# Optimization experiments

Hardware: AMD Instinct MI355X
Metric: run time of the kernel (lower is better)

Reference implementation:

```python
import jax, jax.numpy as jnp
import numpy as np

N = 100000
E = 1600000
F_IN = 128
H = 128
G = 256  # number of graphs
EPS = 1e-5


def setup_inputs() -> dict:
    key = jax.random.key(0)
    ks = jax.random.split(key, 16)
    x = jax.random.normal(ks[0], (N, F_IN), dtype=jnp.float32)
    edge_index = jax.random.randint(ks[1], (2, E), 0, N, dtype=jnp.int64)
    batch = jnp.sort(jax.random.randint(ks[2], (N,), 0, G, dtype=jnp.int64))
    def glorot(k, shape):
        lim = float(np.sqrt(6.0 / (shape[0] + shape[1])))
        return jax.random.uniform(k, shape, jnp.float32, -lim, lim)
    inp = {
        "x": x, "edge_index": edge_index, "batch": batch,
        "W1": glorot(ks[3], (F_IN, H)), "b1": jnp.zeros((H,), jnp.float32),
        "g1": jnp.ones((H,), jnp.float32), "be1": jnp.zeros((H,), jnp.float32),
        "W2": glorot(ks[4], (H, H)), "b2": jnp.zeros((H,), jnp.float32),
        "g2": jnp.ones((H,), jnp.float32), "be2": jnp.zeros((H,), jnp.float32),
        "W3": glorot(ks[5], (H, H)), "b3": jnp.zeros((H,), jnp.float32),
        "g3": jnp.ones((H,), jnp.float32), "be3": jnp.zeros((H,), jnp.float32),
        "Wl": glorot(ks[6], (H, 1)), "bl": jnp.zeros((1,), jnp.float32),
    }
    return inp


def _gcn_precompute(edge_index):
    # add self-loops, compute symmetric norm coefficients (PyG GCNConv default)
    src = jnp.concatenate([edge_index[0], jnp.arange(N, dtype=edge_index.dtype)])
    dst = jnp.concatenate([edge_index[1], jnp.arange(N, dtype=edge_index.dtype)])
    deg = jax.ops.segment_sum(jnp.ones_like(dst, dtype=jnp.float32), dst, num_segments=N)
    dinv = jnp.where(deg > 0, deg ** -0.5, 0.0)
    coef = dinv[src] * dinv[dst]  # [E+N]
    return src, dst, coef


def _gcn_conv(x, src, dst, coef, W, b):
    h = x @ W                                  # [N, H] small GEMM
    msg = h[src] * coef[:, None]               # gather + scale over edges
    out = jax.ops.segment_sum(msg, dst, num_segments=N)  # scatter-add
    return out + b


def _batchnorm(x, g, be):
    # training-mode BN: batch statistics, biased variance (PyTorch semantics)
    mean = jnp.mean(x, axis=0)
    var = jnp.mean(jnp.square(x - mean), axis=0)
    return g * (x - mean) * jax.lax.rsqrt(var + EPS) + be


def reference(x, edge_index, batch, W1, b1, g1, be1, W2, b2, g2, be2,
              W3, b3, g3, be3, Wl, bl):
    src, dst, coef = _gcn_precompute(edge_index)
    h = _gcn_conv(x, src, dst, coef, W1, b1)
    h = jax.nn.relu(_batchnorm(h, g1, be1))  # dropout is identity in eval
    h = _gcn_conv(h, src, dst, coef, W2, b2)
    h = jax.nn.relu(_batchnorm(h, g2, be2))
    h = _gcn_conv(h, src, dst, coef, W3, b3)
    h = jax.nn.relu(_batchnorm(h, g3, be3))
    # global mean pool per graph
    sums = jax.ops.segment_sum(h, batch, num_segments=G)
    cnt = jax.ops.segment_sum(jnp.ones((N,), jnp.float32), batch, num_segments=G)
    pooled = sums / jnp.maximum(cnt, 1.0)[:, None]  # [G, H]
    return pooled @ Wl + bl                          # [G, 1]
```

## Files before the change

### kernel.cpp

```cpp
#include <hip/hip_runtime.h>
#include <hip/hip_bf16.h>

#define N_NODES 100000
#define E_EDGES 1600000
#define FDIM 128
#define NGRAPH 256
#define NPB 256
#define NBUCKET 391
#define SLAB 4800
#define BCHUNK 16384
#define NBINBLK ((E_EDGES + BCHUNK - 1) / BCHUNK)
#define LDSW 136
#define SREP 16

typedef __attribute__((ext_vector_type(8))) short bf16x8;
typedef __attribute__((ext_vector_type(4))) float f32x4;

__device__ __forceinline__ unsigned pack_bf16(float a, float b) {
    unsigned ua = __float_as_uint(a);
    unsigned ub = __float_as_uint(b);
    ua = ua + 0x7fffu + ((ua >> 16) & 1u);
    ub = ub + 0x7fffu + ((ub >> 16) & 1u);
    return (ua >> 16) | (ub & 0xffff0000u);
}
__device__ __forceinline__ unsigned short bf16_1(float a) {
    unsigned ua = __float_as_uint(a);
    ua = ua + 0x7fffu + ((ua >> 16) & 1u);
    return (unsigned short)(ua >> 16);
}
__device__ __forceinline__ float bf_lo(unsigned u) { return __uint_as_float(u << 16); }
__device__ __forceinline__ float bf_hi(unsigned u) { return __uint_as_float(u & 0xffff0000u); }


__global__ void initk(float* __restrict__ statsP, float* __restrict__ sums,
                      int* __restrict__ cursor) {
    int i = blockIdx.x * blockDim.x + threadIdx.x;
    if (i < 3 * SREP * 256) statsP[i] = 0.0f;
    if (i < NGRAPH * FDIM) sums[i] = 0.0f;
    if (i < NBUCKET) cursor[i] = i * SLAB;
}

__global__ __launch_bounds__(256) void bink(const int* __restrict__ ei,
                                            int* __restrict__ cursor,
                                            int* __restrict__ bcsr) {
    __shared__ int hist[NBUCKET];
    __shared__ int base[NBUCKET];
    int t = threadIdx.x;
    for (int b = t; b < NBUCKET; b += 256) hist[b] = 0;
    __syncthreads();
    int e0 = blockIdx.x * BCHUNK;
    int e1 = e0 + BCHUNK; if (e1 > E_EDGES) e1 = E_EDGES;
    for (int e = e0 + t; e < e1; e += 256) {
        atomicAdd(&hist[ei[E_EDGES + e] >> 8], 1);
    }
    __syncthreads();
    for (int b = t; b < NBUCKET; b += 256) {
        int h = hist[b];
        base[b] = h ? atomicAdd(&cursor[b], h) : 0;
        hist[b] = 0;
    }
    __syncthreads();
    for (int e = e0 + t; e < e1; e += 256) {
        int s = ei[e];
        int d = ei[E_EDGES + e];
        int bk = d >> 8;
        int lp = atomicAdd(&hist[bk], 1);
        int pos = base[bk] + lp;
        if (pos < (bk + 1) * SLAB)
            bcsr[pos] = s | ((d & 255) << 17);
    }
}

__global__ __launch_bounds__(256) void sortk(const int* __restrict__ cursor,
                                             int* __restrict__ bcsr,
                                             int* __restrict__ offs,
                                             int* __restrict__ inCnt,
                                             float* __restrict__ dinv) {
    __shared__ int ent[SLAB];
    __shared__ int hist[NPB];
    __shared__ int hcur[NPB];
    __shared__ int htmp[NPB];
    int t = threadIdx.x;
    int bk = blockIdx.x;
    int slab = bk * SLAB;
    int cnt = cursor[bk] - slab;
    if (cnt > SLAB) cnt = SLAB;
    hist[t] = 0;
    __syncthreads();
    for (int i = t; i < cnt; i += 256) {
        int v = bcsr[slab + i];
        ent[i] = v;
        atomicAdd(&hist[v >> 17], 1);
    }
    __syncthreads();
    int myc = hist[t];
    htmp[t] = myc;
    __syncthreads();
    for (int st = 1; st < 256; st <<= 1) {
        int x = htmp[t];
        int y = (t >= st) ? htmp[t - st] : 0;
        __syncthreads();
        htmp[t] = x + y;
        __syncthreads();
    }
    int excl = htmp[t] - myc;
    hist[t] = excl;
    hcur[t] = 0;
    int gn = bk * NPB + t;
    if (gn < N_NODES) {
        inCnt[gn] = myc;
        offs[gn] = slab + excl;
        dinv[gn] = rsqrtf((float)(1 + myc));
    }
    __syncthreads();
    for (int i = t; i < cnt; i += 256) {
        int v = ent[i];
        int dl = v >> 17;
        int lp = atomicAdd(&hcur[dl], 1);
        bcsr[slab + hist[dl] + lp] = v & 0x1FFFF;
    }
}

__global__ __launch_bounds__(256) void transposeW(const float* __restrict__ W1,
                                                  const float* __restrict__ W2,
                                                  const float* __restrict__ W3,
                                                  unsigned short* __restrict__ Wt) {
    int b = blockIdx.x;
    int widx = b >> 3;
    int n0 = (b & 7) * 16;
    const float* W = (widx == 0) ? W1 : (widx == 1) ? W2 : W3;
    unsigned short* dst = Wt + widx * 16384;
    int t = threadIdx.x;
    int n = n0 + (t & 15);
#pragma unroll
    for (int i = 0; i < 8; i++) {
        int k = (t >> 4) + i * 16;
        dst[n * 128 + k] = bf16_1(W[k * 128 + n]);
    }
}


template <int MODE>
__global__ __launch_bounds__(256, 2) void gemmMF(const void* __restrict__ Ain,
                                                 const unsigned short* __restrict__ Wt,
                                                 const float* __restrict__ statsP,
                                                 const float* __restrict__ g,
                                                 const float* __restrict__ be,
                                                 unsigned short* __restrict__ outT) {
    __shared__ unsigned short sA[64 * LDSW];
    __shared__ unsigned short sW[128 * LDSW];
    __shared__ float sScale[FDIM], sBias[FDIM];
    int tid = threadIdx.x;
    if (MODE == 1) {
        if (tid < FDIM) {
            float s = 0.f, q = 0.f;
#pragma unroll
            for (int r = 0; r < SREP; r++) {
                s += statsP[r * 256 + tid];
                q += statsP[r * 256 + 128 + tid];
            }
            float mean = s * (1.0f / N_NODES);
            float var = q * (1.0f / N_NODES) - mean * mean;
            float sc = g[tid] * rsqrtf(var + 1e-5f);
            sScale[tid] = sc;
            sBias[tid] = be[tid] - mean * sc;
        }
        __syncthreads();
    }
    int row0 = blockIdx.x * 64;
    {
        const uint4* Wt4 = (const uint4*)Wt;
#pragma unroll
        for (int i = 0; i < 8; i++) {
            int flat = tid + 256 * i;
            int r = flat >> 4, c8 = flat & 15;
            uint4 v = Wt4[flat];
            *(uint4*)&sW[r * LDSW + c8 * 8] = v;
        }
    }
    if (MODE == 0) {
        const float4* A4 = (const float4*)Ain;
#pragma unroll
        for (int i = 0; i < 8; i++) {
            int flat = tid + 256 * i;
            int r = flat >> 5, c4 = flat & 31;
            int grow = row0 + r;
            float4 v = make_float4(0.f, 0.f, 0.f, 0.f);
            if (grow < N_NODES) v = A4[grow * 32 + c4];
            uint2 p;
            p.x = pack_bf16(v.x, v.y);
            p.y = pack_bf16(v.z, v.w);
            *(uint2*)&sA[r * LDSW + c4 * 4] = p;
        }
    } else {
        const uint2* A2 = (const uint2*)Ain;
#pragma unroll
        for (int i = 0; i < 8; i++) {
            int flat = tid + 256 * i;
            int r = flat >> 5, c4 = flat & 31;
            int grow = row0 + r;
            uint2 u = make_uint2(0u, 0u);
            if (grow < N_NODES) u = A2[grow * 32 + c4];
            int ch = c4 * 4;
            float vx = fmaxf(bf_lo(u.x) * sScale[ch + 0] + sBias[ch + 0], 0.f);
            float vy = fmaxf(bf_hi(u.x) * sScale[ch + 1] + sBias[ch + 1], 0.f);
            float vz = fmaxf(bf_lo(u.y) * sScale[ch + 2] + sBias[ch + 2], 0.f);
            float vw = fmaxf(bf_hi(u.y) * sScale[ch + 3] + sBias[ch + 3], 0.f);
            uint2 p;
            p.x = pack_bf16(vx, vy);
            p.y = pack_bf16(vz, vw);
            *(uint2*)&sA[r * LDSW + c4 * 4] = p;
        }
    }
    __syncthreads();

    int lane = tid & 63;
    int w = tid >> 6;
    int rbase = lane & 15;
    int kgrp = lane >> 4;
    f32x4 acc[4][2];
#pragma unroll
    for (int mf = 0; mf < 4; mf++)
#pragma unroll
        for (int nf = 0; nf < 2; nf++) acc[mf][nf] = (f32x4){0.f, 0.f, 0.f, 0.f};

#pragma unroll
    for (int kk = 0; kk < 4; kk++) {
        int kb = kk * 32 + kgrp * 8;
        bf16x8 af[4], bfr[2];
#pragma unroll
        for (int mf = 0; mf < 4; mf++)
            af[mf] = *(const bf16x8*)&sA[(mf * 16 + rbase) * LDSW + kb];
#pragma unroll
        for (int nf = 0; nf < 2; nf++)
            bfr[nf] = *(const bf16x8*)&sW[(w * 32 + nf * 16 + rbase) * LDSW + kb];
#pragma unroll
        for (int mf = 0; mf < 4; mf++)
#pragma unroll
            for (int nf = 0; nf < 2; nf++)
                acc[mf][nf] = __builtin_amdgcn_mfma_f32_16x16x32_bf16(
                    af[mf], bfr[nf], acc[mf][nf], 0, 0, 0);
    }
#pragma unroll
    for (int mf = 0; mf < 4; mf++) {
#pragma unroll
        for (int nf = 0; nf < 2; nf++) {
            int col = w * 32 + nf * 16 + rbase;
#pragma unroll
            for (int j = 0; j < 4; j++) {
                int grow = row0 + mf * 16 + kgrp * 4 + j;
                if (grow < N_NODES) {
                    outT[(size_t)grow * FDIM + col] = bf16_1(acc[mf][nf][j]);
                }
            }
        }
    }
}


__global__ __launch_bounds__(256) void agg(const unsigned* __restrict__ t,
                                           const int* __restrict__ bcsr,
                                           const int* __restrict__ offs,
                                           const int* __restrict__ inCnt,
                                           const float* __restrict__ dinv,
                                           const float* __restrict__ bias,
                                           unsigned* __restrict__ outH,
                                           float* __restrict__ statsP) {
    int tid = threadIdx.x;
    int lane = tid & 63;
    int wid = tid >> 6;
    const float2* bias2 = (const float2*)bias;
    float2 b = bias2[lane];
    float s0 = 0.f, s1 = 0.f, q0 = 0.f, q1 = 0.f;
    for (int it = 0; it < 8; it++) {
        int node = __builtin_amdgcn_readfirstlane(blockIdx.x * 32 + wid * 8 + it);
        float di = dinv[node];
        unsigned su = t[node * 64 + lane];
        float cs = di * di;
        float a0 = bf_lo(su) * cs;
        float a1 = bf_hi(su) * cs;
        int start = offs[node];
        int cnt = inCnt[node];
        int e = 0;
        for (; e + 4 <= cnt; e += 4) {
            int v0 = bcsr[start + e + 0] & 0x1FFFF;
            int v1 = bcsr[start + e + 1] & 0x1FFFF;
            int v2 = bcsr[start + e + 2] & 0x1FFFF;
            int v3 = bcsr[start + e + 3] & 0x1FFFF;
            float f0 = dinv[v0] * di;
            float f1 = dinv[v1] * di;
            float f2 = dinv[v2] * di;
            float f3 = dinv[v3] * di;
            unsigned u0 = t[v0 * 64 + lane];
            unsigned u1 = t[v1 * 64 + lane];
            unsigned u2 = t[v2 * 64 + lane];
            unsigned u3 = t[v3 * 64 + lane];
            a0 += f0 * bf_lo(u0); a1 += f0 * bf_hi(u0);
            a0 += f1 * bf_lo(u1); a1 += f1 * bf_hi(u1);
            a0 += f2 * bf_lo(u2); a1 += f2 * bf_hi(u2);
            a0 += f3 * bf_lo(u3); a1 += f3 * bf_hi(u3);
        }
        for (; e < cnt; e++) {
            int v = bcsr[start + e] & 0x1FFFF;
            float cf = dinv[v] * di;
            unsigned u = t[v * 64 + lane];
            a0 += cf * bf_lo(u);
            a1 += cf * bf_hi(u);
        }
        a0 += b.x;
        a1 += b.y;
        outH[node * 64 + lane] = pack_bf16(a0, a1);
        s0 += a0; q0 += a0 * a0;
        s1 += a1; q1 += a1 * a1;
    }
    __shared__ float rS0[256], rS1[256], rQ0[256], rQ1[256];
    rS0[tid] = s0; rS1[tid] = s1; rQ0[tid] = q0; rQ1[tid] = q1;
    __syncthreads();
    if (tid < 64) {
        float S0 = 0.f, S1 = 0.f, Q0 = 0.f, Q1 = 0.f;
#pragma unroll
        for (int w = 0; w < 4; w++) {
            S0 += rS0[w * 64 + tid];
            S1 += rS1[w * 64 + tid];
            Q0 += rQ0[w * 64 + tid];
            Q1 += rQ1[w * 64 + tid];
        }
        float* p = statsP + (blockIdx.x & (SREP - 1)) * 256;
        atomicAdd(&p[2 * tid + 0], S0);
        atomicAdd(&p[2 * tid + 1], S1);
        atomicAdd(&p[128 + 2 * tid + 0], Q0);
        atomicAdd(&p[128 + 2 * tid + 1], Q1);
    }
}


__global__ __launch_bounds__(128) void poolsum(const unsigned* __restrict__ h,
                                               const int* __restrict__ batch,
                                               const float* __restrict__ statsP,
                                               const float* __restrict__ g3,
                                               const float* __restrict__ be3,
                                               float* __restrict__ sums) {
    int c = threadIdx.x;
    int base = blockIdx.x * 64;
    float s = 0.f, q = 0.f;
#pragma unroll
    for (int r = 0; r < SREP; r++) {
        s += statsP[r * 256 + c];
        q += statsP[r * 256 + 128 + c];
    }
    float mean = s * (1.0f / N_NODES);
    float var = q * (1.0f / N_NODES) - mean * mean;
    float sc = g3[c] * rsqrtf(var + 1e-5f);
    float bi = be3[c] - mean * sc;
    __shared__ int sb[64];
    if (c < 64) {
        int idx = base + c;
        sb[c] = (idx < N_NODES) ? batch[idx] : -1;
    }
    __syncthreads();
    float acc = 0.f;
    int gcur = sb[0];
    int half = c & 1;
    int cu = c >> 1;
    for (int r = 0; r < 64; r++) {
        int idx = base + r;
        if (idx >= N_NODES) break;
        int gr = sb[r];
        if (gr != gcur) {
            atomicAdd(&sums[gcur * FDIM + c], acc);
            acc = 0.f;
            gcur = gr;
        }
        unsigned u = h[(size_t)idx * 64 + cu];
        float v = half ? bf_hi(u) : bf_lo(u);
        acc += fmaxf(v * sc + bi, 0.f);
    }
    atomicAdd(&sums[gcur * FDIM + c], acc);
}


__global__ __launch_bounds__(128) void finalk(const float* __restrict__ sums,
                                              const int* __restrict__ batch,
                                              const float* __restrict__ Wl,
                                              const float* __restrict__ bl,
                                              float* __restrict__ out) {
    int g = blockIdx.x;
    int c = threadIdx.x;
    int lo = 0, hi = N_NODES;
    while (lo < hi) { int m = (lo + hi) >> 1; if (batch[m] < g) lo = m + 1; else hi = m; }
    int start = lo;
    lo = start; hi = N_NODES;
    while (lo < hi) { int m = (lo + hi) >> 1; if (batch[m] < g + 1) lo = m + 1; else hi = m; }
    int cnt = lo - start;
    float v = sums[g * FDIM + c] / fmaxf((float)cnt, 1.0f) * Wl[c];
    __shared__ float red[FDIM];
    red[c] = v;
    __syncthreads();
    for (int st = 64; st > 0; st >>= 1) {
        if (c < st) red[c] += red[c + st];
        __syncthreads();
    }
    if (c == 0) out[g] = red[0] + bl[0];
}


extern "C" void kernel_launch(void* const* d_in, const int* in_sizes, int n_in,
                              void* d_out, int out_size, void* d_ws, size_t ws_size,
                              hipStream_t stream) {
    const float* x  = (const float*)d_in[0];
    const int* ei   = (const int*)d_in[1];
    const int* batch = (const int*)d_in[2];
    const float* W1 = (const float*)d_in[3];
    const float* b1 = (const float*)d_in[4];
    const float* g1 = (const float*)d_in[5];
    const float* be1 = (const float*)d_in[6];
    const float* W2 = (const float*)d_in[7];
    const float* b2 = (const float*)d_in[8];
    const float* g2 = (const float*)d_in[9];
    const float* be2 = (const float*)d_in[10];
    const float* W3 = (const float*)d_in[11];
    const float* b3 = (const float*)d_in[12];
    const float* g3 = (const float*)d_in[13];
    const float* be3 = (const float*)d_in[14];
    const float* Wl = (const float*)d_in[15];
    const float* bl = (const float*)d_in[16];
    float* out = (float*)d_out;

    char* ws = (char*)d_ws;
    size_t off = 0;
    auto alloc = [&](size_t bytes) -> char* {
        char* p = ws + off;
        off = (off + bytes + 255) & ~(size_t)255;
        return p;
    };
    float* dinv    = (float*)alloc(N_NODES * 4);
    int* offs      = (int*)alloc(N_NODES * 4);
    int* inCnt     = (int*)alloc(N_NODES * 4);
    int* cursor    = (int*)alloc(NBUCKET * 4);
    int* bcsr      = (int*)alloc((size_t)NBUCKET * SLAB * 4);
    float* statsP  = (float*)alloc(3 * SREP * 256 * 4);
    float* sums    = (float*)alloc(NGRAPH * FDIM * 4);
    unsigned short* Wt = (unsigned short*)alloc(3 * 16384 * 2);
    unsigned short* T16 = (unsigned short*)alloc((size_t)N_NODES * FDIM * 2);
    unsigned* H    = (unsigned*)alloc((size_t)N_NODES * 64 * 4);

    const int nb_nodes = (N_NODES + 255) / 256;
    const int nb_gemm = (N_NODES + 63) / 64;
    const int nb_agg = N_NODES / 32;
    const int nb_pool = (N_NODES + 63) / 64;

    initk<<<nb_nodes, 256, 0, stream>>>(statsP, sums, cursor);
    bink<<<NBINBLK, 256, 0, stream>>>(ei, cursor, bcsr);
    sortk<<<NBUCKET, 256, 0, stream>>>(cursor, bcsr, offs, inCnt, dinv);
    transposeW<<<24, 256, 0, stream>>>(W1, W2, W3, Wt);

    gemmMF<0><<<nb_gemm, 256, 0, stream>>>(x, Wt, nullptr, nullptr, nullptr, T16);
    agg<<<nb_agg, 256, 0, stream>>>((const unsigned*)T16, bcsr, offs, inCnt, dinv, b1, H, statsP);

    gemmMF<1><<<nb_gemm, 256, 0, stream>>>(H, Wt + 16384, statsP, g1, be1, T16);
    agg<<<nb_agg, 256, 0, stream>>>((const unsigned*)T16, bcsr, offs, inCnt, dinv, b2, H, statsP + SREP * 256);

    gemmMF<1><<<nb_gemm, 256, 0, stream>>>(H, Wt + 32768, statsP + SREP * 256, g2, be2, T16);
    agg<<<nb_agg, 256, 0, stream>>>((const unsigned*)T16, bcsr, offs, inCnt, dinv, b3, H, statsP + 2 * SREP * 256);

    poolsum<<<nb_pool, 128, 0, stream>>>(H, batch, statsP + 2 * SREP * 256, g3, be3, sums);
    finalk<<<NGRAPH, 128, 0, stream>>>(sums, batch, Wl, bl, out);
}
```

Measured before the change: 392.8 us.

## Precompute edge coefficients and split wave into two half-waves per edge in agg

Adds a coefk pass that stores each CSR entry as a (source, dinv[s]*dinv[d]) pair, so agg no longer does a dependent dinv gather per edge. agg now has each half-wave handle alternate edges with 8-byte feature loads, unrolls eight edges per half-wave to keep more gathers in flight, and combines the halves with a cross-lane shuffle. The binning chunk size is also reduced to spread bink over more blocks. The cost is an extra kernel and an 8-byte-per-edge array, plus shuffle and reduction overhead.

```diff
diff --git a/kernel.cpp b/kernel.cpp
--- a/kernel.cpp
+++ b/kernel.cpp
@@ -8,7 +8,7 @@
 #define NPB 256
 #define NBUCKET 391
 #define SLAB 4800
-#define BCHUNK 16384
+#define BCHUNK 2048
 #define NBINBLK ((E_EDGES + BCHUNK - 1) / BCHUNK)
 #define LDSW 136
 #define SREP 16
@@ -117,7 +117,23 @@
         int v = ent[i];
         int dl = v >> 17;
         int lp = atomicAdd(&hcur[dl], 1);
-        bcsr[slab + hist[dl] + lp] = v & 0x1FFFF;
+        bcsr[slab + hist[dl] + lp] = v;
+    }
+}
+
+__global__ __launch_bounds__(256) void coefk(const int* __restrict__ cursor,
+                                             const int* __restrict__ bcsr,
+                                             const float* __restrict__ dinv,
+                                             int2* __restrict__ csr2) {
+    int bk = blockIdx.x;
+    int slab = bk * SLAB;
+    int cnt = cursor[bk] - slab;
+    if (cnt > SLAB) cnt = SLAB;
+    for (int i = threadIdx.x; i < cnt; i += 256) {
+        int v = bcsr[slab + i];
+        int s = v & 0x1FFFF;
+        int d = bk * NPB + (v >> 17);
+        csr2[slab + i] = make_int2(s, __float_as_int(dinv[s] * dinv[d]));
     }
 }
 
@@ -258,78 +274,91 @@
 }
 
 
-__global__ __launch_bounds__(256) void agg(const unsigned* __restrict__ t,
-                                           const int* __restrict__ bcsr,
+__global__ __launch_bounds__(256) void agg(const uint2* __restrict__ t2,
+                                           const int2* __restrict__ csr2,
                                            const int* __restrict__ offs,
                                            const int* __restrict__ inCnt,
                                            const float* __restrict__ dinv,
                                            const float* __restrict__ bias,
-                                           unsigned* __restrict__ outH,
+                                           uint2* __restrict__ outH2,
                                            float* __restrict__ statsP) {
     int tid = threadIdx.x;
     int lane = tid & 63;
+    int sub = lane & 31;
+    int grp = lane >> 5;
     int wid = tid >> 6;
-    const float2* bias2 = (const float2*)bias;
-    float2 b = bias2[lane];
-    float s0 = 0.f, s1 = 0.f, q0 = 0.f, q1 = 0.f;
+    float4 b4 = ((const float4*)bias)[sub];
+    float s0 = 0.f, s1 = 0.f, s2 = 0.f, s3 = 0.f;
+    float q0 = 0.f, q1 = 0.f, q2 = 0.f, q3 = 0.f;
     for (int it = 0; it < 8; it++) {
         int node = __builtin_amdgcn_readfirstlane(blockIdx.x * 32 + wid * 8 + it);
         float di = dinv[node];
-        unsigned su = t[node * 64 + lane];
-        float cs = di * di;
-        float a0 = bf_lo(su) * cs;
-        float a1 = bf_hi(su) * cs;
+        float cs = (grp == 0) ? di * di : 0.0f;
+        uint2 su = t2[node * 32 + sub];
+        float a0 = bf_lo(su.x) * cs, a1 = bf_hi(su.x) * cs;
+        float a2 = bf_lo(su.y) * cs, a3 = bf_hi(su.y) * cs;
         int start = offs[node];
         int cnt = inCnt[node];
         int e = 0;
-        for (; e + 4 <= cnt; e += 4) {
-            int v0 = bcsr[start + e + 0] & 0x1FFFF;
-            int v1 = bcsr[start + e + 1] & 0x1FFFF;
-            int v2 = bcsr[start + e + 2] & 0x1FFFF;
-            int v3 = bcsr[start + e + 3] & 0x1FFFF;
-            float f0 = dinv[v0] * di;
-            float f1 = dinv[v1] * di;
-            float f2 = dinv[v2] * di;
-            float f3 = dinv[v3] * di;
-            unsigned u0 = t[v0 * 64 + lane];
-            unsigned u1 = t[v1 * 64 + lane];
-            unsigned u2 = t[v2 * 64 + lane];
-            unsigned u3 = t[v3 * 64 + lane];
-            a0 += f0 * bf_lo(u0); a1 += f0 * bf_hi(u0);
-            a0 += f1 * bf_lo(u1); a1 += f1 * bf_hi(u1);
-            a0 += f2 * bf_lo(u2); a1 += f2 * bf_hi(u2);
-            a0 += f3 * bf_lo(u3); a1 += f3 * bf_hi(u3);
-        }
-        for (; e < cnt; e++) {
-            int v = bcsr[start + e] & 0x1FFFF;
-            float cf = dinv[v] * di;
-            unsigned u = t[v * 64 + lane];
-            a0 += cf * bf_lo(u);
-            a1 += cf * bf_hi(u);
-        }
-        a0 += b.x;
-        a1 += b.y;
-        outH[node * 64 + lane] = pack_bf16(a0, a1);
-        s0 += a0; q0 += a0 * a0;
-        s1 += a1; q1 += a1 * a1;
-    }
-    __shared__ float rS0[256], rS1[256], rQ0[256], rQ1[256];
-    rS0[tid] = s0; rS1[tid] = s1; rQ0[tid] = q0; rQ1[tid] = q1;
-    __syncthreads();
-    if (tid < 64) {
-        float S0 = 0.f, S1 = 0.f, Q0 = 0.f, Q1 = 0.f;
-#pragma unroll
-        for (int w = 0; w < 4; w++) {
-            S0 += rS0[w * 64 + tid];
-            S1 += rS1[w * 64 + tid];
-            Q0 += rQ0[w * 64 + tid];
-            Q1 += rQ1[w * 64 + tid];
-        }
+        for (; e + 16 <= cnt; e += 16) {
+            int2 E[8];
+            uint2 U[8];
+#pragma unroll
+            for (int k = 0; k < 8; k++) E[k] = csr2[start + e + 2 * k + grp];
+#pragma unroll
+            for (int k = 0; k < 8; k++) U[k] = t2[E[k].x * 32 + sub];
+#pragma unroll
+            for (int k = 0; k < 8; k++) {
+                float f = __int_as_float(E[k].y);
+                a0 += f * bf_lo(U[k].x); a1 += f * bf_hi(U[k].x);
+                a2 += f * bf_lo(U[k].y); a3 += f * bf_hi(U[k].y);
+            }
+        }
+        for (; e + 2 <= cnt; e += 2) {
+            int2 E = csr2[start + e + grp];
+            uint2 U = t2[E.x * 32 + sub];
+            float f = __int_as_float(E.y);
+            a0 += f * bf_lo(U.x); a1 += f * bf_hi(U.x);
+            a2 += f * bf_lo(U.y); a3 += f * bf_hi(U.y);
+        }
+        if (e < cnt) {
+            int2 E = csr2[start + e];
+            uint2 U = t2[E.x * 32 + sub];
+            float f = (grp == 0) ? __int_as_float(E.y) : 0.0f;
+            a0 += f * bf_lo(U.x); a1 += f * bf_hi(U.x);
+            a2 += f * bf_lo(U.y); a3 += f * bf_hi(U.y);
+        }
+        a0 += __shfl_xor(a0, 32, 64);
+        a1 += __shfl_xor(a1, 32, 64);
+        a2 += __shfl_xor(a2, 32, 64);
+        a3 += __shfl_xor(a3, 32, 64);
+        a0 += b4.x; a1 += b4.y; a2 += b4.z; a3 += b4.w;
+        if (grp == 0) {
+            uint2 p;
+            p.x = pack_bf16(a0, a1);
+            p.y = pack_bf16(a2, a3);
+            outH2[node * 32 + sub] = p;
+            s0 += a0; q0 += a0 * a0;
+            s1 += a1; q1 += a1 * a1;
+            s2 += a2; q2 += a2 * a2;
+            s3 += a3; q3 += a3 * a3;
+        }
+    }
+    __shared__ float sS[4 * 128], sQ[4 * 128];
+    if (grp == 0) {
+        int chb = wid * 128 + 4 * sub;
+        sS[chb + 0] = s0; sQ[chb + 0] = q0;
+        sS[chb + 1] = s1; sQ[chb + 1] = q1;
+        sS[chb + 2] = s2; sQ[chb + 2] = q2;
+        sS[chb + 3] = s3; sQ[chb + 3] = q3;
+    }
+    __syncthreads();
+    if (tid < 128) {
+        float S = sS[tid] + sS[128 + tid] + sS[256 + tid] + sS[384 + tid];
+        float Q = sQ[tid] + sQ[128 + tid] + sQ[256 + tid] + sQ[384 + tid];
         float* p = statsP + (blockIdx.x & (SREP - 1)) * 256;
-        atomicAdd(&p[2 * tid + 0], S0);
-        atomicAdd(&p[2 * tid + 1], S1);
-        atomicAdd(&p[128 + 2 * tid + 0], Q0);
-        atomicAdd(&p[128 + 2 * tid + 1], Q1);
+        atomicAdd(&p[tid], S);
+        atomicAdd(&p[128 + tid], Q);
     }
 }
 
@@ -438,6 +467,7 @@
     int* inCnt     = (int*)alloc(N_NODES * 4);
     int* cursor    = (int*)alloc(NBUCKET * 4);
     int* bcsr      = (int*)alloc((size_t)NBUCKET * SLAB * 4);
+    int2* csr2     = (int2*)alloc((size_t)NBUCKET * SLAB * 8);
     float* statsP  = (float*)alloc(3 * SREP * 256 * 4);
     float* sums    = (float*)alloc(NGRAPH * FDIM * 4);
     unsigned short* Wt = (unsigned short*)alloc(3 * 16384 * 2);
@@ -452,16 +482,20 @@
     initk<<<nb_nodes, 256, 0, stream>>>(statsP, sums, cursor);
     bink<<<NBINBLK, 256, 0, stream>>>(ei, cursor, bcsr);
     sortk<<<NBUCKET, 256, 0, stream>>>(cursor, bcsr, offs, inCnt, dinv);
+    coefk<<<NBUCKET, 256, 0, stream>>>(cursor, bcsr, dinv, csr2);
     transposeW<<<24, 256, 0, stream>>>(W1, W2, W3, Wt);
 
     gemmMF<0><<<nb_gemm, 256, 0, stream>>>(x, Wt, nullptr, nullptr, nullptr, T16);
-    agg<<<nb_agg, 256, 0, stream>>>((const unsigned*)T16, bcsr, offs, inCnt, dinv, b1, H, statsP);
+    agg<<<nb_agg, 256, 0, stream>>>((const uint2*)T16, csr2, offs, inCnt, dinv, b1,
+                                    (uint2*)H, statsP);
 
     gemmMF<1><<<nb_gemm, 256, 0, stream>>>(H, Wt + 16384, statsP, g1, be1, T16);
-    agg<<<nb_agg, 256, 0, stream>>>((const unsigned*)T16, bcsr, offs, inCnt, dinv, b2, H, statsP + SREP * 256);
+    agg<<<nb_agg, 256, 0, stream>>>((const uint2*)T16, csr2, offs, inCnt, dinv, b2,
+                                    (uint2*)H, statsP + SREP * 256);
 
     gemmMF<1><<<nb_gemm, 256, 0, stream>>>(H, Wt + 32768, statsP + SREP * 256, g2, be2, T16);
-    agg<<<nb_agg, 256, 0, stream>>>((const unsigned*)T16, bcsr, offs, inCnt, dinv, b3, H, statsP + 2 * SREP * 256);
+    agg<<<nb_agg, 256, 0, stream>>>((const uint2*)T16, csr2, offs, inCnt, dinv, b3,
+                                    (uint2*)H, statsP + 2 * SREP * 256);
 
     poolsum<<<nb_pool, 128, 0, stream>>>(H, batch, statsP + 2 * SREP * 256, g3, be3, sums);
     finalk<<<NGRAPH, 128, 0, stream>>>(sums, batch, Wl, bl, out);
```

Result: slower. 459.5 us (+17.0%).

## Precompute fp16 edge coefficients into packed CSR and shard aggregation by feature

Applied to the files above, without the earlier changes.

Adds a coefk kernel that packs each edge's source index together with an fp16 normalization coefficient into one 32-bit word. The separate dinv gather per edge in aggregation goes away. The agg kernel now splits the 128 features into 8 shards over separate blocks, and each wavefront handles 8 edges in parallel with 8 lanes per edge, finishing with a cross-lane shuffle reduction. The edge binning chunk size is also reduced. This trades a full feature-row read per edge for narrower 32-byte segments, gives more parallelism per node, and lowers coefficient precision to fp16.

```diff
diff --git a/kernel.cpp b/kernel.cpp
--- a/kernel.cpp
+++ b/kernel.cpp
@@ -1,5 +1,6 @@
 #include <hip/hip_runtime.h>
 #include <hip/hip_bf16.h>
+#include <hip/hip_fp16.h>
 
 #define N_NODES 100000
 #define E_EDGES 1600000
@@ -8,10 +9,11 @@
 #define NPB 256
 #define NBUCKET 391
 #define SLAB 4800
-#define BCHUNK 16384
+#define BCHUNK 2048
 #define NBINBLK ((E_EDGES + BCHUNK - 1) / BCHUNK)
 #define LDSW 136
 #define SREP 16
+#define NSHARD 8
 
 typedef __attribute__((ext_vector_type(8))) short bf16x8;
 typedef __attribute__((ext_vector_type(4))) float f32x4;
@@ -117,7 +119,25 @@
         int v = ent[i];
         int dl = v >> 17;
         int lp = atomicAdd(&hcur[dl], 1);
-        bcsr[slab + hist[dl] + lp] = v & 0x1FFFF;
+        bcsr[slab + hist[dl] + lp] = v;
+    }
+}
+
+__global__ __launch_bounds__(256) void coefk(const int* __restrict__ cursor,
+                                             const int* __restrict__ bcsr,
+                                             const float* __restrict__ dinv,
+                                             unsigned* __restrict__ csrp) {
+    int bk = blockIdx.x;
+    int slab = bk * SLAB;
+    int cnt = cursor[bk] - slab;
+    if (cnt > SLAB) cnt = SLAB;
+    for (int i = threadIdx.x; i < cnt; i += 256) {
+        int v = bcsr[slab + i];
+        int s = v & 0x1FFFF;
+        int d = bk * NPB + (v >> 17);
+        float coef = dinv[s] * dinv[d];
+        unsigned hb = (unsigned)__half_as_ushort(__float2half(coef));
+        csrp[slab + i] = (unsigned)s | (hb << 17);
     }
 }
 
@@ -259,7 +279,7 @@
 
 
 __global__ __launch_bounds__(256) void agg(const unsigned* __restrict__ t,
-                                           const int* __restrict__ bcsr,
+                                           const unsigned* __restrict__ csrp,
                                            const int* __restrict__ offs,
                                            const int* __restrict__ inCnt,
                                            const float* __restrict__ dinv,
@@ -269,67 +289,58 @@
     int tid = threadIdx.x;
     int lane = tid & 63;
     int wid = tid >> 6;
+    int shard = blockIdx.x & (NSHARD - 1);
+    int nbase = (blockIdx.x >> 3) * 32;
+    int esub = lane >> 3;
+    int ch = lane & 7;
+    int tb = shard * 8 + ch;
     const float2* bias2 = (const float2*)bias;
-    float2 b = bias2[lane];
+    float2 b = bias2[tb];
     float s0 = 0.f, s1 = 0.f, q0 = 0.f, q1 = 0.f;
     for (int it = 0; it < 8; it++) {
-        int node = __builtin_amdgcn_readfirstlane(blockIdx.x * 32 + wid * 8 + it);
+        int node = __builtin_amdgcn_readfirstlane(nbase + wid * 8 + it);
         float di = dinv[node];
-        unsigned su = t[node * 64 + lane];
-        float cs = di * di;
-        float a0 = bf_lo(su) * cs;
-        float a1 = bf_hi(su) * cs;
         int start = offs[node];
         int cnt = inCnt[node];
-        int e = 0;
-        for (; e + 4 <= cnt; e += 4) {
-            int v0 = bcsr[start + e + 0] & 0x1FFFF;
-            int v1 = bcsr[start + e + 1] & 0x1FFFF;
-            int v2 = bcsr[start + e + 2] & 0x1FFFF;
-            int v3 = bcsr[start + e + 3] & 0x1FFFF;
-            float f0 = dinv[v0] * di;
-            float f1 = dinv[v1] * di;
-            float f2 = dinv[v2] * di;
-            float f3 = dinv[v3] * di;
-            unsigned u0 = t[v0 * 64 + lane];
-            unsigned u1 = t[v1 * 64 + lane];
-            unsigned u2 = t[v2 * 64 + lane];
-            unsigned u3 = t[v3 * 64 + lane];
+        float a0 = 0.f, a1 = 0.f;
+        for (int e = 0; e < cnt; e += 16) {
+            int i0 = e + esub;
+            int i1 = e + 8 + esub;
+            unsigned v0 = (i0 < cnt) ? __builtin_nontemporal_load(&csrp[start + i0]) : 0u;
+            unsigned v1 = (i1 < cnt) ? __builtin_nontemporal_load(&csrp[start + i1]) : 0u;
+            unsigned u0 = t[(v0 & 0x1FFFF) * 64 + tb];
+            unsigned u1 = t[(v1 & 0x1FFFF) * 64 + tb];
+            float f0 = __half2float(__ushort_as_half((unsigned short)(v0 >> 17)));
+            float f1 = __half2float(__ushort_as_half((unsigned short)(v1 >> 17)));
             a0 += f0 * bf_lo(u0); a1 += f0 * bf_hi(u0);
             a0 += f1 * bf_lo(u1); a1 += f1 * bf_hi(u1);
-            a0 += f2 * bf_lo(u2); a1 += f2 * bf_hi(u2);
-            a0 += f3 * bf_lo(u3); a1 += f3 * bf_hi(u3);
-        }
-        for (; e < cnt; e++) {
-            int v = bcsr[start + e] & 0x1FFFF;
-            float cf = dinv[v] * di;
-            unsigned u = t[v * 64 + lane];
-            a0 += cf * bf_lo(u);
-            a1 += cf * bf_hi(u);
-        }
-        a0 += b.x;
-        a1 += b.y;
-        outH[node * 64 + lane] = pack_bf16(a0, a1);
-        s0 += a0; q0 += a0 * a0;
-        s1 += a1; q1 += a1 * a1;
-    }
-    __shared__ float rS0[256], rS1[256], rQ0[256], rQ1[256];
-    rS0[tid] = s0; rS1[tid] = s1; rQ0[tid] = q0; rQ1[tid] = q1;
-    __syncthreads();
-    if (tid < 64) {
-        float S0 = 0.f, S1 = 0.f, Q0 = 0.f, Q1 = 0.f;
-#pragma unroll
-        for (int w = 0; w < 4; w++) {
-            S0 += rS0[w * 64 + tid];
-            S1 += rS1[w * 64 + tid];
-            Q0 += rQ0[w * 64 + tid];
-            Q1 += rQ1[w * 64 + tid];
-        }
-        float* p = statsP + (blockIdx.x & (SREP - 1)) * 256;
-        atomicAdd(&p[2 * tid + 0], S0);
-        atomicAdd(&p[2 * tid + 1], S1);
-        atomicAdd(&p[128 + 2 * tid + 0], Q0);
-        atomicAdd(&p[128 + 2 * tid + 1], Q1);
+        }
+        a0 += __shfl_xor(a0, 8, 64);  a1 += __shfl_xor(a1, 8, 64);
+        a0 += __shfl_xor(a0, 16, 64); a1 += __shfl_xor(a1, 16, 64);
+        a0 += __shfl_xor(a0, 32, 64); a1 += __shfl_xor(a1, 32, 64);
+        unsigned su = t[node * 64 + tb];
+        float cs = di * di;
+        a0 += cs * bf_lo(su) + b.x;
+        a1 += cs * bf_hi(su) + b.y;
+        if (esub == 0) {
+            outH[node * 64 + tb] = pack_bf16(a0, a1);
+            s0 += a0; q0 += a0 * a0;
+            s1 += a1; q1 += a1 * a1;
+        }
+    }
+    __shared__ float sS[64], sQ[64];
+    if (esub == 0) {
+        sS[wid * 16 + 2 * ch + 0] = s0; sQ[wid * 16 + 2 * ch + 0] = q0;
+        sS[wid * 16 + 2 * ch + 1] = s1; sQ[wid * 16 + 2 * ch + 1] = q1;
+    }
+    __syncthreads();
+    if (tid < 16) {
+        float S = sS[tid] + sS[16 + tid] + sS[32 + tid] + sS[48 + tid];
+        float Q = sQ[tid] + sQ[16 + tid] + sQ[32 + tid] + sQ[48 + tid];
+        int gch = shard * 16 + tid;
+        float* p = statsP + ((blockIdx.x >> 3) & (SREP - 1)) * 256;
+        atomicAdd(&p[gch], S);
+        atomicAdd(&p[128 + gch], Q);
     }
 }
 
@@ -438,6 +449,7 @@
     int* inCnt     = (int*)alloc(N_NODES * 4);
     int* cursor    = (int*)alloc(NBUCKET * 4);
     int* bcsr      = (int*)alloc((size_t)NBUCKET * SLAB * 4);
+    unsigned* csrp = (unsigned*)alloc((size_t)NBUCKET * SLAB * 4);
     float* statsP  = (float*)alloc(3 * SREP * 256 * 4);
     float* sums    = (float*)alloc(NGRAPH * FDIM * 4);
     unsigned short* Wt = (unsigned short*)alloc(3 * 16384 * 2);
@@ -446,22 +458,23 @@
 
     const int nb_nodes = (N_NODES + 255) / 256;
     const int nb_gemm = (N_NODES + 63) / 64;
-    const int nb_agg = N_NODES / 32;
+    const int nb_agg = (N_NODES / 32) * NSHARD;
     const int nb_pool = (N_NODES + 63) / 64;
 
     initk<<<nb_nodes, 256, 0, stream>>>(statsP, sums, cursor);
     bink<<<NBINBLK, 256, 0, stream>>>(ei, cursor, bcsr);
     sortk<<<NBUCKET, 256, 0, stream>>>(cursor, bcsr, offs, inCnt, dinv);
+    coefk<<<NBUCKET, 256, 0, stream>>>(cursor, bcsr, dinv, csrp);
     transposeW<<<24, 256, 0, stream>>>(W1, W2, W3, Wt);
 
     gemmMF<0><<<nb_gemm, 256, 0, stream>>>(x, Wt, nullptr, nullptr, nullptr, T16);
-    agg<<<nb_agg, 256, 0, stream>>>((const unsigned*)T16, bcsr, offs, inCnt, dinv, b1, H, statsP);
+    agg<<<nb_agg, 256, 0, stream>>>((const unsigned*)T16, csrp, offs, inCnt, dinv, b1, H, statsP);
 
     gemmMF<1><<<nb_gemm, 256, 0, stream>>>(H, Wt + 16384, statsP, g1, be1, T16);
-    agg<<<nb_agg, 256, 0, stream>>>((const unsigned*)T16, bcsr, offs, inCnt, dinv, b2, H, statsP + SREP * 256);
+    agg<<<nb_agg, 256, 0, stream>>>((const unsigned*)T16, csrp, offs, inCnt, dinv, b2, H, statsP + SREP * 256);
 
     gemmMF<1><<<nb_gemm, 256, 0, stream>>>(H, Wt + 32768, statsP + SREP * 256, g2, be2, T16);
-    agg<<<nb_agg, 256, 0, stream>>>((const unsigned*)T16, bcsr, offs, inCnt, dinv, b3, H, statsP + 2 * SREP * 256);
+    agg<<<nb_agg, 256, 0, stream>>>((const unsigned*)T16, csrp, offs, inCnt, dinv, b3, H, statsP + 2 * SREP * 256);
 
     poolsum<<<nb_pool, 128, 0, stream>>>(H, batch, statsP + 2 * SREP * 256, g3, be3, sums);
     finalk<<<NGRAPH, 128, 0, stream>>>(sums, batch, Wl, bl, out);
```

Result: slower. 960.2 us (+144.4%).
